# Performance work log

Measured on AMD Instinct MI355X. Metric: run time of the kernel, lower is better.

The kernel has to match this reference:

```python
import jax, jax.numpy as jnp
import numpy as np

B, N_PER, DEG = 1024, 256, 16
N = B * N_PER            # 262144 total nodes
E = B * N_PER * DEG      # 4194304 edges
F_IN, H, K, C = 7, 64, 50, 2


def setup_inputs() -> dict:
    key = jax.random.key(0)
    ks = jax.random.split(key, 16)
    rng = np.random.default_rng(0)
    # within-graph random edges: nodes of graph g occupy [g*N_PER, (g+1)*N_PER)
    offs = np.repeat(np.arange(B, dtype=np.int64) * N_PER, N_PER * DEG)
    src = offs + rng.integers(0, N_PER, size=E)
    dst = offs + rng.integers(0, N_PER, size=E)
    edge_index = jnp.asarray(np.stack([src, dst]), dtype=jnp.int64)
    batch = jnp.repeat(jnp.arange(B, dtype=jnp.int64), N_PER)
    sc = lambda fan: 1.0 / np.sqrt(fan)
    return {
        'x': jax.random.normal(ks[0], (N, F_IN), jnp.float32),
        'W1a': jax.random.normal(ks[1], (F_IN, H), jnp.float32) * sc(F_IN),
        'b1a': jnp.zeros((H,), jnp.float32),
        'W1b': jax.random.normal(ks[2], (H, H), jnp.float32) * sc(H),
        'b1b': jnp.zeros((H,), jnp.float32),
        'Wp': jax.random.normal(ks[3], (H, K), jnp.float32) * sc(H),
        'bp': jnp.zeros((K,), jnp.float32),
        'W2a': jax.random.normal(ks[4], (H, H), jnp.float32) * sc(H),
        'b2a': jnp.zeros((H,), jnp.float32),
        'W2b': jax.random.normal(ks[5], (H, H), jnp.float32) * sc(H),
        'b2b': jnp.zeros((H,), jnp.float32),
        'Wl': jax.random.normal(ks[6], (H, C), jnp.float32) * sc(H),
        'bl': jnp.zeros((C,), jnp.float32),
        'edge_index': edge_index,
        'batch': batch,
    }


def reference(x, W1a, b1a, W1b, b1b, Wp, bp, W2a, b2a, W2b, b2b, Wl, bl,
              edge_index, batch):
    src, dst = edge_index[0], edge_index[1]
    # --- sparse GINConv (eps=0): MLP(x + sum_{j in N(i)} x_j) ---
    agg = jnp.zeros_like(x).at[dst].add(x[src])          # scatter-add over edges
    h = jax.nn.relu((x + agg) @ W1a + b1a) @ W1b + b1b   # [N, H]
    # --- densify per graph (equal-size contiguous graphs) ---
    xd = h.reshape(B, N_PER, H)                          # [B, n, H]
    g = src // N_PER
    si = src % N_PER
    di = dst % N_PER
    A = jnp.zeros((B, N_PER, N_PER), x.dtype).at[g, si, di].add(1.0)
    # --- BNPool-style soft cluster pooling ---
    S = jax.nn.softmax(xd @ Wp + bp, axis=-1)            # [B, n, K]
    xp = jnp.einsum('bnk,bnd->bkd', S, xd)               # [B, K, H]
    AS = jnp.einsum('bnm,bmk->bnk', A, S)
    Ap = jnp.einsum('bnk,bnl->bkl', S, AS)               # [B, K, K]
    SSt = jnp.einsum('bnk,bmk->bnm', S, S)
    link_loss = jnp.sqrt(jnp.sum((A - SSt) ** 2)) / A.size
    ent_loss = -jnp.mean(jnp.sum(S * jnp.log(S + 1e-15), axis=-1))
    aux_loss = link_loss + ent_loss
    # --- DenseGINConv (eps=0): MLP(x + A @ x) ---
    h2 = xp + jnp.einsum('bkl,bld->bkd', Ap, xp)
    h2 = jax.nn.relu(h2 @ W2a + b2a) @ W2b + b2b         # [B, K, H]
    # --- mean pool over clusters + classifier ---
    logits = h2.mean(axis=1) @ Wl + bl                   # [B, C]
    return jax.nn.log_softmax(logits, axis=-1), aux_loss
```

## Files before the change

### kernel.cpp

```cpp
#include <hip/hip_runtime.h>
#include <math.h>

#define NG   1024
#define NP   256
#define EPG  4096
#define ETOT 4194304
#define FIN  7
#define HD   64
#define KC   50
#define FST  72
#define TST  264
#define TSC  0.00390625f
#define TSCI 256.0f

#define SW_ST(k, n)  ((k) * 256 + ((n) ^ (((k) & 7) << 3)))
#define SW_AW(r, w)  ((r) * 128 + ((w) ^ (((r) & 7) << 2)))
#define SW_AH(r, h)  ((r) * 256 + ((h) ^ (((r) & 7) << 3)))


typedef __attribute__((ext_vector_type(8))) _Float16 v8h;
typedef __attribute__((ext_vector_type(4))) float v4f;

__device__ __align__(16) _Float16 g_W1bT[HD * HD];
__device__ __align__(16) _Float16 g_WWT[HD * HD];
__device__ __align__(16) _Float16 g_W2aT[HD * HD];
__device__ __align__(16) _Float16 g_W2bT[HD * HD];
__device__ float g_bP[HD];

__global__ void kw_conv(const float* __restrict__ W1b, const float* __restrict__ Wp,
                        const float* __restrict__ W2a, const float* __restrict__ W2b,
                        const float* __restrict__ b1b, const float* __restrict__ bp,
                        float* __restrict__ ws) {
    const int b = blockIdx.x, tid = threadIdx.x;
    if (b == 0 && tid < 4) ws[tid] = 0.f;
    {
        int i = b * 256 + tid;
        int d = i >> 6, j = i & 63;
        g_W1bT[i] = (_Float16)W1b[j * HD + d];
        g_W2aT[i] = (_Float16)W2a[j * HD + d];
        g_W2bT[i] = (_Float16)W2b[j * HD + d];
    }
    {
        int k = b * 4 + (tid >> 6), j = tid & 63;
        float acc = 0.f;
        if (k < KC) {
            for (int d = 0; d < HD; ++d)
                acc += W1b[j * HD + d] * Wp[d * KC + k];
        }
        g_WWT[k * HD + j] = (_Float16)acc;
    }
    if (tid < 4) {
        int k = b * 4 + tid;
        float a = 0.f;
        if (k < KC) {
            for (int d = 0; d < HD; ++d) a += b1b[d] * Wp[d * KC + k];
            a += bp[k];
        }
        g_bP[k] = a;
    }
}

__global__ void finalize_k(const float* __restrict__ ws, float* __restrict__ out) {
    if (threadIdx.x == 0) {
        float num = ws[0] - 2.f * ws[2] + ws[3];
        float link = sqrtf(fmaxf(num, 0.f)) / 67108864.0f;
        float ent  = -ws[1] / 262144.0f;
        out[2048] = link + ent;
    }
}

__device__ __forceinline__ float blockReduceN(float v, float* red, int nw) {
    __syncthreads();
    #pragma unroll
    for (int o = 32; o > 0; o >>= 1) v += __shfl_down(v, o);
    if ((threadIdx.x & 63) == 0) red[threadIdx.x >> 6] = v;
    __syncthreads();
    float r = 0.f;
    if (threadIdx.x == 0) {
        for (int i = 0; i < nw; ++i) r += red[i];
    }
    return r;
}

__device__ __forceinline__ void blockReduce3(float& a, float& b, float& c,
                                             float* red) {
    __syncthreads();
    #pragma unroll
    for (int o = 32; o > 0; o >>= 1) {
        a += __shfl_down(a, o);
        b += __shfl_down(b, o);
        c += __shfl_down(c, o);
    }
    const int wid = threadIdx.x >> 6;
    if ((threadIdx.x & 63) == 0) {
        red[wid * 3] = a; red[wid * 3 + 1] = b; red[wid * 3 + 2] = c;
    }
    __syncthreads();
    if (threadIdx.x == 0) {
        float ra = 0.f, rb = 0.f, rc = 0.f;
        for (int i = 0; i < 16; ++i) {
            ra += red[i * 3]; rb += red[i * 3 + 1]; rc += red[i * 3 + 2];
        }
        a = ra; b = rb; c = rc;
    }
}

__launch_bounds__(1024, 1)
__global__ void mega(const int* __restrict__ esrc, const int* __restrict__ edst,
                     const float* __restrict__ x,
                     const float* __restrict__ W1a, const float* __restrict__ b1a,
                     const float* __restrict__ b1b,
                     const float* __restrict__ b2a, const float* __restrict__ b2b,
                     const float* __restrict__ Wl,  const float* __restrict__ bl,
                     float* __restrict__ out, float* __restrict__ ws)
{
    __shared__ __align__(16) _Float16 ST[64 * 256];
    __shared__ __align__(16) _Float16 xagg[NP * 8];
    __shared__ __align__(16) union {
        struct {
            unsigned char ssi[EPG];
            float xt8[NP * 8];
            unsigned int hist[256], cur[256], roff[NP + 1];
        } k1;
        struct {
            _Float16 t1b[NP * FST];
            _Float16 t1T[HD * TST];
        } k2;
        struct {
            unsigned int cnt[64 * 128];
            _Float16 T1T[64 * FST];
        } a;
        struct {
            _Float16 Apf_tf[64 * FST];
            _Float16 xpT[64 * FST];
            _Float16 h2f[64 * FST];
        } b;
    } u;
    __shared__ float cs[64];
    __shared__ float red[48];

    const int g = blockIdx.x, tid = threadIdx.x;
    const int lane = tid & 63, wid = tid >> 6;
    const int l15 = lane & 15, quad = lane >> 4, fko = quad * 8;
    const int mt = (wid >> 2) << 4, nt = (wid & 3) << 4;

    for (int i = tid; i < 64 * 128; i += 1024) ((unsigned int*)ST)[i] = 0u;
    if (tid < 256) u.k1.hist[tid] = 0u;
    __syncthreads();

    unsigned int cellr[4];
    #pragma unroll
    for (int j = 0; j < 4; ++j) {
        int e = tid + j * 1024;
        int s = esrc[g * EPG + e] & (NP - 1);
        int d = edst[g * EPG + e] & (NP - 1);
        cellr[j] = (unsigned)((s << 8) | d);
        atomicAdd(&u.k1.hist[d], 1u);
    }
    for (int i = tid; i < NP * 8; i += 1024) {
        int n = i >> 3, f = i & 7;
        u.k1.xt8[i] = (f < FIN) ? x[g * NP * FIN + n * FIN + f] : 0.f;
    }
    __syncthreads();

    if (wid == 0) {
        unsigned carry = 0;
        for (int c = 0; c < 4; ++c) {
            unsigned v = u.k1.hist[c * 64 + lane];
            unsigned s = v;
            #pragma unroll
            for (int o = 1; o < 64; o <<= 1) {
                unsigned t = __shfl_up(s, o);
                if (lane >= o) s += t;
            }
            unsigned excl = s - v + carry;
            u.k1.roff[c * 64 + lane] = excl;
            u.k1.cur[c * 64 + lane] = excl;
            carry += __shfl(s, 63);
        }
        if (lane == 0) u.k1.roff[NP] = EPG;
    }
    __syncthreads();

    #pragma unroll
    for (int j = 0; j < 4; ++j) {
        unsigned c = cellr[j];
        unsigned p2 = atomicAdd(&u.k1.cur[c & 255u], 1u);
        u.k1.ssi[p2] = (unsigned char)(c >> 8);
    }
    __syncthreads();

    {
        const int gi = tid >> 3, f = tid & 7;
        for (int n = gi; n < NP; n += 128) {
            int beg = u.k1.roff[n], end = u.k1.roff[n + 1];
            float a = u.k1.xt8[n * 8 + f];
            for (int e = beg; e < end; ++e)
                a += u.k1.xt8[u.k1.ssi[e] * 8 + f];
            xagg[n * 8 + f] = (_Float16)a;
        }
    }
    __syncthreads();

    {
        float w1r[FIN];
        #pragma unroll
        for (int f = 0; f < FIN; ++f) w1r[f] = W1a[f * HD + lane];
        float b1r = b1a[lane];
        for (int it = 0; it < 16; ++it) {
            int n = it * 16 + wid;
            float a = b1r;
            #pragma unroll
            for (int f = 0; f < FIN; ++f)
                a += (float)xagg[n * 8 + f] * w1r[f];
            _Float16 tv = (_Float16)fmaxf(a, 0.f);
            u.k2.t1b[n * FST + lane] = tv;
            u.k2.t1T[lane * TST + n] = tv;
        }
    }
    __syncthreads();

    float entL = 0.f;
    {
        const int r16 = wid << 4;
        v4f pa[4];
        #pragma unroll
        for (int c = 0; c < 4; ++c) {
            v4f acc = {0.f, 0.f, 0.f, 0.f};
            #pragma unroll
            for (int ks = 0; ks < 2; ++ks) {
                v8h af = *(const v8h*)&u.k2.t1b[(r16 + l15) * FST + ks * 32 + fko];
                v8h bf = *(const v8h*)&g_WWT[(c * 16 + l15) * HD + ks * 32 + fko];
                acc = __builtin_amdgcn_mfma_f32_16x16x32_f16(af, bf, acc, 0, 0, 0);
            }
            pa[c] = acc;
        }
        float bv[4]; bool valid[4];
        #pragma unroll
        for (int c = 0; c < 4; ++c) {
            int col = c * 16 + l15;
            bv[c] = g_bP[col];
            valid[c] = col < KC;
        }
        #pragma unroll
        for (int r = 0; r < 4; ++r) {
            float pv[4];
            #pragma unroll
            for (int c = 0; c < 4; ++c)
                pv[c] = valid[c] ? (pa[c][r] + bv[c]) : -INFINITY;
            float m = fmaxf(fmaxf(pv[0], pv[1]), fmaxf(pv[2], pv[3]));
            #pragma unroll
            for (int o = 8; o > 0; o >>= 1) m = fmaxf(m, __shfl_xor(m, o));
            float e[4], Z = 0.f;
            #pragma unroll
            for (int c = 0; c < 4; ++c) {
                e[c] = valid[c] ? __expf(pv[c] - m) : 0.f;
                Z += e[c];
            }
            #pragma unroll
            for (int o = 8; o > 0; o >>= 1) Z += __shfl_xor(Z, o);
            float zi = 1.f / Z, lZ = __logf(Z);
            int row = r16 + quad * 4 + r;
            #pragma unroll
            for (int c = 0; c < 4; ++c) {
                if (valid[c]) {
                    float s = e[c] * zi;
                    ST[SW_ST(c * 16 + l15, row)] = (_Float16)s;
                    entL += s * (pv[c] - m);
                }
            }
            if (l15 == 0) entL -= lZ;
        }
    }
    __syncthreads();

    v4f spa = {0.f, 0.f, 0.f, 0.f};
    {
        const int ar = mt + l15, br = nt + l15;
        #pragma unroll
        for (int ks = 0; ks < 8; ++ks) {
            int ko = ks * 32 + fko;
            v8h af = *(const v8h*)&ST[SW_ST(ar, ko)];
            v8h bf = *(const v8h*)&u.k2.t1T[br * TST + ko];
            spa = __builtin_amdgcn_mfma_f32_16x16x32_f16(af, bf, spa, 0, 0, 0);
        }
    }
    {
        _Float16* SPb = u.k2.t1b;
        int c = nt + l15;
        #pragma unroll
        for (int r = 0; r < 4; ++r)
            SPb[(mt + quad * 4 + r) * FST + c] = (_Float16)spa[r];
    }
    {
        int k = tid >> 4, q = tid & 15;
        float v = 0.f;
        #pragma unroll
        for (int i = 0; i < 16; ++i) v += (float)ST[SW_ST(k, q * 16 + i)];
        #pragma unroll
        for (int o = 8; o > 0; o >>= 1) v += __shfl_xor(v, o);
        if (q == 0) cs[k] = v;
    }
    {
        float rE = blockReduceN(entL, red, 16);
        if (tid == 0) atomicAdd(&ws[1], rE);
    }

    v4f axp;
    {
        const int d = nt + l15;
        float bv = b1b[d];
        #pragma unroll
        for (int r = 0; r < 4; ++r) axp[r] = cs[mt + quad * 4 + r] * bv;
        #pragma unroll
        for (int ks = 0; ks < 2; ++ks) {
            v8h af = *(const v8h*)&u.k2.t1b[(mt + l15) * FST + ks * 32 + fko];
            v8h bf = *(const v8h*)&g_W1bT[(nt + l15) * HD + ks * 32 + fko];
            axp = __builtin_amdgcn_mfma_f32_16x16x32_f16(af, bf, axp, 0, 0, 0);
        }
    }
    __syncthreads();

    float sumA2 = 0.f;
    v4f ap = {0.f, 0.f, 0.f, 0.f};
    v4f ag = {0.f, 0.f, 0.f, 0.f};

    for (int ch = 0; ch < 4; ++ch) {
        for (int i = tid; i < 64 * 128; i += 1024) u.a.cnt[i] = 0u;
        __syncthreads();

        int rlo = ch << 6;
        #pragma unroll
        for (int j = 0; j < 4; ++j) {
            unsigned c = cellr[j];
            int sr = (int)(c >> 8) - rlo;
            if ((unsigned)sr < 64u) {
                int d = c & 255u;
                atomicAdd(&u.a.cnt[SW_AW(sr, d >> 1)],
                          (d & 1) ? 0x10000u : 1u);
            }
        }
        __syncthreads();

        for (int i = tid; i < 64 * 128; i += 1024) {
            unsigned v = u.a.cnt[i];
            float m0 = (float)(v & 0xffffu), m1 = (float)(v >> 16);
            sumA2 += m0 * m0 + m1 * m1;
            union { unsigned uu; _Float16 h[2]; } cv;
            cv.h[0] = (_Float16)m0; cv.h[1] = (_Float16)m1;
            u.a.cnt[i] = cv.uu;
        }
        __syncthreads();

        const _Float16* Af = (const _Float16*)u.a.cnt;

        {
            const int ar = mt + l15, br = nt + l15;
            v4f acc = {0.f, 0.f, 0.f, 0.f};
            #pragma unroll
            for (int ks = 0; ks < 8; ++ks) {
                v8h af = *(const v8h*)&Af[SW_AH(ar, ks * 32 + fko)];
                v8h bf = *(const v8h*)&ST[SW_ST(br, ks * 32 + fko)];
                acc = __builtin_amdgcn_mfma_f32_16x16x32_f16(af, bf, acc, 0, 0, 0);
            }
            int c = nt + l15;
            #pragma unroll
            for (int r = 0; r < 4; ++r)
                u.a.T1T[c * FST + mt + quad * 4 + r] = (_Float16)acc[r];
        }
        __syncthreads();

        {
            const int ar = mt + l15, br = nt + l15;
            #pragma unroll
            for (int ks = 0; ks < 2; ++ks) {
                int ko = (ch << 6) + ks * 32 + fko;
                v8h af = *(const v8h*)&ST[SW_ST(ar, ko)];
                v8h bt = *(const v8h*)&u.a.T1T[br * FST + ks * 32 + fko];
                v8h bs = *(const v8h*)&ST[SW_ST(br, ko)];
                ap = __builtin_amdgcn_mfma_f32_16x16x32_f16(af, bt, ap, 0, 0, 0);
                ag = __builtin_amdgcn_mfma_f32_16x16x32_f16(af, bs, ag, 0, 0, 0);
            }
        }
        __syncthreads();
    }

    float tr = 0.f, g2 = 0.f;
    {
        int c = nt + l15;
        #pragma unroll
        for (int r = 0; r < 4; ++r) {
            int k = mt + quad * 4 + r;
            u.b.Apf_tf[k * FST + c] = (_Float16)ap[r];
            u.b.xpT[c * FST + k] = (_Float16)axp[r];
            if (k < KC && c < KC) {
                if (k == c) tr += ap[r];
                g2 += ag[r] * ag[r];
            }
        }
    }

    blockReduce3(sumA2, tr, g2, red);
    if (tid == 0) {
        atomicAdd(&ws[0], sumA2);
        atomicAdd(&ws[2], tr);
        atomicAdd(&ws[3], g2);
    }
    __syncthreads();

    {
        v4f hacc = axp;
        #pragma unroll
        for (int ks = 0; ks < 2; ++ks) {
            v8h af = *(const v8h*)&u.b.Apf_tf[(mt + l15) * FST + ks * 32 + fko];
            v8h bf = *(const v8h*)&u.b.xpT[(nt + l15) * FST + ks * 32 + fko];
            hacc = __builtin_amdgcn_mfma_f32_16x16x32_f16(af, bf, hacc, 0, 0, 0);
        }
        int d = nt + l15;
        #pragma unroll
        for (int r = 0; r < 4; ++r)
            u.b.h2f[(mt + quad * 4 + r) * FST + d] = (_Float16)(hacc[r] * TSC);
    }
    __syncthreads();

    {
        float bv = b2a[nt + l15] * TSC;
        v4f tacc = {bv, bv, bv, bv};
        #pragma unroll
        for (int ks = 0; ks < 2; ++ks) {
            v8h af = *(const v8h*)&u.b.h2f[(mt + l15) * FST + ks * 32 + fko];
            v8h bf = *(const v8h*)&g_W2aT[(nt + l15) * 64 + ks * 32 + fko];
            tacc = __builtin_amdgcn_mfma_f32_16x16x32_f16(af, bf, tacc, 0, 0, 0);
        }
        int d2 = nt + l15;
        #pragma unroll
        for (int r = 0; r < 4; ++r)
            u.b.Apf_tf[(mt + quad * 4 + r) * FST + d2] = (_Float16)fmaxf(tacc[r], 0.f);
    }
    __syncthreads();

    float l0 = 0.f, l1 = 0.f;
    {
        v4f oacc = {0.f, 0.f, 0.f, 0.f};
        #pragma unroll
        for (int ks = 0; ks < 2; ++ks) {
            v8h af = *(const v8h*)&u.b.Apf_tf[(mt + l15) * FST + ks * 32 + fko];
            v8h bf = *(const v8h*)&g_W2bT[(nt + l15) * 64 + ks * 32 + fko];
            oacc = __builtin_amdgcn_mfma_f32_16x16x32_f16(af, bf, oacc, 0, 0, 0);
        }
        int j = nt + l15;
        float bv = b2b[j];
        float wl0 = Wl[j * 2], wl1 = Wl[j * 2 + 1];
        #pragma unroll
        for (int r = 0; r < 4; ++r) {
            int k = mt + quad * 4 + r;
            if (k < KC) {
                float h3v = oacc[r] * TSCI + bv;
                l0 += h3v * wl0; l1 += h3v * wl1;
            }
        }
    }

    float dummy = 0.f;
    blockReduce3(l0, l1, dummy, red);
    if (tid == 0) {
        float g0 = bl[0] + l0 * (1.f / KC);
        float g1 = bl[1] + l1 * (1.f / KC);
        float mm = fmaxf(g0, g1);
        float lse = mm + logf(expf(g0 - mm) + expf(g1 - mm));
        out[2 * g]     = g0 - lse;
        out[2 * g + 1] = g1 - lse;
    }
}

extern "C" void kernel_launch(void* const* d_in, const int* in_sizes, int n_in,
                              void* d_out, int out_size, void* d_ws, size_t ws_size,
                              hipStream_t stream) {
    const float* x    = (const float*)d_in[0];
    const float* W1a  = (const float*)d_in[1];
    const float* b1a  = (const float*)d_in[2];
    const float* W1b  = (const float*)d_in[3];
    const float* b1b  = (const float*)d_in[4];
    const float* Wp   = (const float*)d_in[5];
    const float* bp   = (const float*)d_in[6];
    const float* W2a  = (const float*)d_in[7];
    const float* b2a  = (const float*)d_in[8];
    const float* W2b  = (const float*)d_in[9];
    const float* b2b  = (const float*)d_in[10];
    const float* Wl   = (const float*)d_in[11];
    const float* bl   = (const float*)d_in[12];
    const int*   eidx = (const int*)d_in[13];
    float* out = (float*)d_out;
    float* ws  = (float*)d_ws;

    kw_conv<<<16, 256, 0, stream>>>(W1b, Wp, W2a, W2b, b1b, bp, ws);
    mega<<<NG, 1024, 0, stream>>>(eidx, eidx + ETOT, x,
                                  W1a, b1a, b1b,
                                  b2a, b2b, Wl, bl, out, ws);
    finalize_k<<<1, 64, 0, stream>>>(ws, out);
}
```

Measured before the change: 254.8 us.

## Fold weight prep into main kernel and halve adjacency chunk passes

Removes the separate weight-conversion kernel. Each block now converts and transposes W1b/W2a/W2b/Wp into LDS and computes the fused W1b·Wp product and bias with an MFMA, replacing the prep launch with a memset. The adjacency count chunking goes from four 64-row passes to two 128-row passes with a larger count buffer, which cuts the number of barriers and zeroing passes. The cost is that every block repeats the weight conversion and uses more LDS. A fast-math log/exp is also used in the final log-softmax.

```diff
diff --git a/kernel.cpp b/kernel.cpp
--- a/kernel.cpp
+++ b/kernel.cpp
@@ -10,6 +10,7 @@
 #define KC   50
 #define FST  72
 #define TST  264
+#define AST2 132
 #define TSC  0.00390625f
 #define TSCI 256.0f
 
@@ -20,45 +21,6 @@
 
 typedef __attribute__((ext_vector_type(8))) _Float16 v8h;
 typedef __attribute__((ext_vector_type(4))) float v4f;
-
-__device__ __align__(16) _Float16 g_W1bT[HD * HD];
-__device__ __align__(16) _Float16 g_WWT[HD * HD];
-__device__ __align__(16) _Float16 g_W2aT[HD * HD];
-__device__ __align__(16) _Float16 g_W2bT[HD * HD];
-__device__ float g_bP[HD];
-
-__global__ void kw_conv(const float* __restrict__ W1b, const float* __restrict__ Wp,
-                        const float* __restrict__ W2a, const float* __restrict__ W2b,
-                        const float* __restrict__ b1b, const float* __restrict__ bp,
-                        float* __restrict__ ws) {
-    const int b = blockIdx.x, tid = threadIdx.x;
-    if (b == 0 && tid < 4) ws[tid] = 0.f;
-    {
-        int i = b * 256 + tid;
-        int d = i >> 6, j = i & 63;
-        g_W1bT[i] = (_Float16)W1b[j * HD + d];
-        g_W2aT[i] = (_Float16)W2a[j * HD + d];
-        g_W2bT[i] = (_Float16)W2b[j * HD + d];
-    }
-    {
-        int k = b * 4 + (tid >> 6), j = tid & 63;
-        float acc = 0.f;
-        if (k < KC) {
-            for (int d = 0; d < HD; ++d)
-                acc += W1b[j * HD + d] * Wp[d * KC + k];
-        }
-        g_WWT[k * HD + j] = (_Float16)acc;
-    }
-    if (tid < 4) {
-        int k = b * 4 + tid;
-        float a = 0.f;
-        if (k < KC) {
-            for (int d = 0; d < HD; ++d) a += b1b[d] * Wp[d * KC + k];
-            a += bp[k];
-        }
-        g_bP[k] = a;
-    }
-}
 
 __global__ void finalize_k(const float* __restrict__ ws, float* __restrict__ out) {
     if (threadIdx.x == 0) {
@@ -109,13 +71,20 @@
 __global__ void mega(const int* __restrict__ esrc, const int* __restrict__ edst,
                      const float* __restrict__ x,
                      const float* __restrict__ W1a, const float* __restrict__ b1a,
-                     const float* __restrict__ b1b,
-                     const float* __restrict__ b2a, const float* __restrict__ b2b,
+                     const float* __restrict__ W1b, const float* __restrict__ b1b,
+                     const float* __restrict__ Wp,  const float* __restrict__ bp,
+                     const float* __restrict__ W2a, const float* __restrict__ b2a,
+                     const float* __restrict__ W2b, const float* __restrict__ b2b,
                      const float* __restrict__ Wl,  const float* __restrict__ bl,
                      float* __restrict__ out, float* __restrict__ ws)
 {
     __shared__ __align__(16) _Float16 ST[64 * 256];
     __shared__ __align__(16) _Float16 xagg[NP * 8];
+    __shared__ __align__(16) _Float16 W1bT[64 * FST];
+    __shared__ __align__(16) _Float16 WWT[64 * FST];
+    __shared__ __align__(16) _Float16 W2aT[64 * FST];
+    __shared__ __align__(16) _Float16 W2bT[64 * FST];
+    __shared__ float bPl[64];
     __shared__ __align__(16) union {
         struct {
             unsigned char ssi[EPG];
@@ -123,12 +92,17 @@
             unsigned int hist[256], cur[256], roff[NP + 1];
         } k1;
         struct {
+            unsigned char pad[16384];
+            _Float16 WpT_s[64 * FST];
+            _Float16 W1bN[64 * FST];
+        } w;
+        struct {
             _Float16 t1b[NP * FST];
             _Float16 t1T[HD * TST];
         } k2;
         struct {
-            unsigned int cnt[64 * 128];
-            _Float16 T1T[64 * FST];
+            unsigned int cnt[128 * 128];
+            _Float16 T1T[64 * AST2];
         } a;
         struct {
             _Float16 Apf_tf[64 * FST];
@@ -145,6 +119,7 @@
     const int mt = (wid >> 2) << 4, nt = (wid & 3) << 4;
 
     for (int i = tid; i < 64 * 128; i += 1024) ((unsigned int*)ST)[i] = 0u;
+    for (int i = tid; i < 64 * FST / 2; i += 1024) ((unsigned int*)u.w.WpT_s)[i] = 0u;
     if (tid < 256) u.k1.hist[tid] = 0u;
     __syncthreads();
 
@@ -161,6 +136,19 @@
         int n = i >> 3, f = i & 7;
         u.k1.xt8[i] = (f < FIN) ? x[g * NP * FIN + n * FIN + f] : 0.f;
     }
+    #pragma unroll
+    for (int j = 0; j < 4; ++j) {
+        int i = tid + j * 1024;
+        int a0 = i >> 6, b0 = i & 63;
+        W1bT[b0 * FST + a0] = (_Float16)W1b[i];
+        u.w.W1bN[a0 * FST + b0] = (_Float16)W1b[i];
+        W2aT[b0 * FST + a0] = (_Float16)W2a[i];
+        W2bT[b0 * FST + a0] = (_Float16)W2b[i];
+    }
+    for (int i = tid; i < HD * KC; i += 1024) {
+        int h2 = i / KC, k = i - h2 * KC;
+        u.w.WpT_s[k * FST + h2] = (_Float16)Wp[i];
+    }
     __syncthreads();
 
     if (wid == 0) {
@@ -179,6 +167,30 @@
             carry += __shfl(s, 63);
         }
         if (lane == 0) u.k1.roff[NP] = EPG;
+    }
+    {
+        v4f acc = {0.f, 0.f, 0.f, 0.f};
+        #pragma unroll
+        for (int ks = 0; ks < 2; ++ks) {
+            v8h af = *(const v8h*)&u.w.WpT_s[(mt + l15) * FST + ks * 32 + fko];
+            v8h bf = *(const v8h*)&u.w.W1bN[(nt + l15) * FST + ks * 32 + fko];
+            acc = __builtin_amdgcn_mfma_f32_16x16x32_f16(af, bf, acc, 0, 0, 0);
+        }
+        #pragma unroll
+        for (int r = 0; r < 4; ++r)
+            WWT[(mt + quad * 4 + r) * FST + nt + l15] = (_Float16)acc[r];
+    }
+    {
+        int k = tid >> 4, q = tid & 15;
+        float v = 0.f;
+        #pragma unroll
+        for (int d0 = 0; d0 < 4; ++d0) {
+            int d = q * 4 + d0;
+            v += b1b[d] * (float)u.w.WpT_s[k * FST + d];
+        }
+        #pragma unroll
+        for (int o = 8; o > 0; o >>= 1) v += __shfl_xor(v, o);
+        if (q == 0) bPl[k] = v + ((k < KC) ? bp[k] : 0.f);
     }
     __syncthreads();
 
@@ -230,7 +242,7 @@
             #pragma unroll
             for (int ks = 0; ks < 2; ++ks) {
                 v8h af = *(const v8h*)&u.k2.t1b[(r16 + l15) * FST + ks * 32 + fko];
-                v8h bf = *(const v8h*)&g_WWT[(c * 16 + l15) * HD + ks * 32 + fko];
+                v8h bf = *(const v8h*)&WWT[(c * 16 + l15) * FST + ks * 32 + fko];
                 acc = __builtin_amdgcn_mfma_f32_16x16x32_f16(af, bf, acc, 0, 0, 0);
             }
             pa[c] = acc;
@@ -239,7 +251,7 @@
         #pragma unroll
         for (int c = 0; c < 4; ++c) {
             int col = c * 16 + l15;
-            bv[c] = g_bP[col];
+            bv[c] = bPl[col];
             valid[c] = col < KC;
         }
         #pragma unroll
@@ -315,7 +327,7 @@
         #pragma unroll
         for (int ks = 0; ks < 2; ++ks) {
             v8h af = *(const v8h*)&u.k2.t1b[(mt + l15) * FST + ks * 32 + fko];
-            v8h bf = *(const v8h*)&g_W1bT[(nt + l15) * HD + ks * 32 + fko];
+            v8h bf = *(const v8h*)&W1bT[(nt + l15) * FST + ks * 32 + fko];
             axp = __builtin_amdgcn_mfma_f32_16x16x32_f16(af, bf, axp, 0, 0, 0);
         }
     }
@@ -325,16 +337,16 @@
     v4f ap = {0.f, 0.f, 0.f, 0.f};
     v4f ag = {0.f, 0.f, 0.f, 0.f};
 
-    for (int ch = 0; ch < 4; ++ch) {
-        for (int i = tid; i < 64 * 128; i += 1024) u.a.cnt[i] = 0u;
-        __syncthreads();
-
-        int rlo = ch << 6;
+    for (int i = tid; i < 128 * 128; i += 1024) u.a.cnt[i] = 0u;
+    __syncthreads();
+
+    for (int ch = 0; ch < 2; ++ch) {
+        int rlo = ch << 7;
         #pragma unroll
         for (int j = 0; j < 4; ++j) {
             unsigned c = cellr[j];
             int sr = (int)(c >> 8) - rlo;
-            if ((unsigned)sr < 64u) {
+            if ((unsigned)sr < 128u) {
                 int d = c & 255u;
                 atomicAdd(&u.a.cnt[SW_AW(sr, d >> 1)],
                           (d & 1) ? 0x10000u : 1u);
@@ -342,7 +354,7 @@
         }
         __syncthreads();
 
-        for (int i = tid; i < 64 * 128; i += 1024) {
+        for (int i = tid; i < 128 * 128; i += 1024) {
             unsigned v = u.a.cnt[i];
             float m0 = (float)(v & 0xffffu), m1 = (float)(v >> 16);
             sumA2 += m0 * m0 + m1 * m1;
@@ -354,33 +366,38 @@
 
         const _Float16* Af = (const _Float16*)u.a.cnt;
 
+        #pragma unroll
+        for (int tt = 0; tt < 2; ++tt) {
+            int t = wid + tt * 16;
+            int mt3 = (t >> 2) << 4, nt3 = (t & 3) << 4;
+            v4f acc = {0.f, 0.f, 0.f, 0.f};
+            #pragma unroll
+            for (int ks = 0; ks < 8; ++ks) {
+                v8h af = *(const v8h*)&Af[SW_AH(mt3 + l15, ks * 32 + fko)];
+                v8h bf = *(const v8h*)&ST[SW_ST(nt3 + l15, ks * 32 + fko)];
+                acc = __builtin_amdgcn_mfma_f32_16x16x32_f16(af, bf, acc, 0, 0, 0);
+            }
+            int c = nt3 + l15;
+            #pragma unroll
+            for (int r = 0; r < 4; ++r)
+                u.a.T1T[c * AST2 + mt3 + quad * 4 + r] = (_Float16)acc[r];
+        }
+        __syncthreads();
+
         {
             const int ar = mt + l15, br = nt + l15;
-            v4f acc = {0.f, 0.f, 0.f, 0.f};
-            #pragma unroll
-            for (int ks = 0; ks < 8; ++ks) {
-                v8h af = *(const v8h*)&Af[SW_AH(ar, ks * 32 + fko)];
-                v8h bf = *(const v8h*)&ST[SW_ST(br, ks * 32 + fko)];
-                acc = __builtin_amdgcn_mfma_f32_16x16x32_f16(af, bf, acc, 0, 0, 0);
-            }
-            int c = nt + l15;
-            #pragma unroll
-            for (int r = 0; r < 4; ++r)
-                u.a.T1T[c * FST + mt + quad * 4 + r] = (_Float16)acc[r];
-        }
-        __syncthreads();
-
-        {
-            const int ar = mt + l15, br = nt + l15;
-            #pragma unroll
-            for (int ks = 0; ks < 2; ++ks) {
-                int ko = (ch << 6) + ks * 32 + fko;
+            #pragma unroll
+            for (int ks = 0; ks < 4; ++ks) {
+                int ko = (ch << 7) + ks * 32 + fko;
                 v8h af = *(const v8h*)&ST[SW_ST(ar, ko)];
-                v8h bt = *(const v8h*)&u.a.T1T[br * FST + ks * 32 + fko];
+                v8h bt = *(const v8h*)&u.a.T1T[br * AST2 + ks * 32 + fko];
                 v8h bs = *(const v8h*)&ST[SW_ST(br, ko)];
                 ap = __builtin_amdgcn_mfma_f32_16x16x32_f16(af, bt, ap, 0, 0, 0);
                 ag = __builtin_amdgcn_mfma_f32_16x16x32_f16(af, bs, ag, 0, 0, 0);
             }
+        }
+        if (ch < 1) {
+            for (int i = tid; i < 128 * 128; i += 1024) u.a.cnt[i] = 0u;
         }
         __syncthreads();
     }
@@ -429,7 +446,7 @@
         #pragma unroll
         for (int ks = 0; ks < 2; ++ks) {
             v8h af = *(const v8h*)&u.b.h2f[(mt + l15) * FST + ks * 32 + fko];
-            v8h bf = *(const v8h*)&g_W2aT[(nt + l15) * 64 + ks * 32 + fko];
+            v8h bf = *(const v8h*)&W2aT[(nt + l15) * FST + ks * 32 + fko];
             tacc = __builtin_amdgcn_mfma_f32_16x16x32_f16(af, bf, tacc, 0, 0, 0);
         }
         int d2 = nt + l15;
@@ -445,7 +462,7 @@
         #pragma unroll
         for (int ks = 0; ks < 2; ++ks) {
             v8h af = *(const v8h*)&u.b.Apf_tf[(mt + l15) * FST + ks * 32 + fko];
-            v8h bf = *(const v8h*)&g_W2bT[(nt + l15) * 64 + ks * 32 + fko];
+            v8h bf = *(const v8h*)&W2bT[(nt + l15) * FST + ks * 32 + fko];
             oacc = __builtin_amdgcn_mfma_f32_16x16x32_f16(af, bf, oacc, 0, 0, 0);
         }
         int j = nt + l15;
@@ -467,7 +484,7 @@
         float g0 = bl[0] + l0 * (1.f / KC);
         float g1 = bl[1] + l1 * (1.f / KC);
         float mm = fmaxf(g0, g1);
-        float lse = mm + logf(expf(g0 - mm) + expf(g1 - mm));
+        float lse = mm + __logf(__expf(g0 - mm) + __expf(g1 - mm));
         out[2 * g]     = g0 - lse;
         out[2 * g + 1] = g1 - lse;
     }
@@ -493,9 +510,9 @@
     float* out = (float*)d_out;
     float* ws  = (float*)d_ws;
 
-    kw_conv<<<16, 256, 0, stream>>>(W1b, Wp, W2a, W2b, b1b, bp, ws);
+    hipMemsetAsync(ws, 0, 4 * sizeof(float), stream);
     mega<<<NG, 1024, 0, stream>>>(eidx, eidx + ETOT, x,
-                                  W1a, b1a, b1b,
-                                  b2a, b2b, Wl, bl, out, ws);
+                                  W1a, b1a, W1b, b1b, Wp, bp,
+                                  W2a, b2a, W2b, b2b, Wl, bl, out, ws);
     finalize_k<<<1, 64, 0, stream>>>(ws, out);
 }
```

Result: faster. 239.7 us (-5.9%).
